# Optimization experiments

Hardware: AMD Instinct MI355X
Metric: run time of the kernel (lower is better)

## Reference

```python
import jax, jax.numpy as jnp
import numpy as np

EMB = 1024
HEADS = 16
DK = EMB // HEADS
EPS = 1e-5


def setup_inputs() -> dict:
    key = jax.random.key(0)
    ks = jax.random.split(key, 7)
    s_in = 1.0 / np.sqrt(EMB)
    return {
        "x": jax.random.normal(ks[0], (4, 2048, EMB), dtype=jnp.float32),
        "W_qkv": jax.random.uniform(ks[1], (EMB, 3 * EMB), jnp.float32, -s_in, s_in),
        "b_qkv": jax.random.uniform(ks[2], (3 * EMB,), jnp.float32, -s_in, s_in),
        "W_out": jax.random.uniform(ks[3], (EMB, EMB), jnp.float32, -s_in, s_in),
        "b_out": jax.random.uniform(ks[4], (EMB,), jnp.float32, -s_in, s_in),
        "gamma": jnp.ones((EMB,), jnp.float32),
        "beta": jnp.zeros((EMB,), jnp.float32),
    }


def reference(x, W_qkv, b_qkv, W_out, b_out, gamma, beta):
    B, T, D = x.shape
    qkv = x @ W_qkv + b_qkv                      # [B,T,3D]
    q, k, v = jnp.split(qkv, 3, axis=-1)
    # [B,T,D] -> [B,H,T,dk]
    def heads(t):
        return t.reshape(B, T, HEADS, DK).transpose(0, 2, 1, 3)
    q, k, v = heads(q), heads(k), heads(v)
    scores = jnp.einsum("bhtd,bhsd->bhts", q, k) / np.sqrt(DK)
    attn = jax.nn.softmax(scores, axis=-1)
    out = jnp.einsum("bhts,bhsd->bhtd", attn, v)  # [B,H,T,dk]
    out = out.transpose(0, 2, 1, 3).reshape(B, T, D)
    out = out @ W_out + b_out
    res = x + out
    mu = jnp.mean(res, axis=-1, keepdims=True)
    var = jnp.mean((res - mu) ** 2, axis=-1, keepdims=True)
    return (res - mu) / jnp.sqrt(var + EPS) * gamma + beta
```

## Files before the change

kernel.cpp:

```cpp
#include <hip/hip_runtime.h>

#define B_ 4
#define T_ 2048
#define D_ 1024
#define H_ 16
#define DK_ 64
#define M_ (B_*T_)

typedef __bf16 bf16;
typedef __bf16 bf16x8 __attribute__((ext_vector_type(8)));
typedef __bf16 bf16x4 __attribute__((ext_vector_type(4)));
typedef short s16x4 __attribute__((ext_vector_type(4)));
typedef float f32x4 __attribute__((ext_vector_type(4)));

__device__ __forceinline__ f32x4 zero4() { f32x4 v = {0.f, 0.f, 0.f, 0.f}; return v; }

__device__ __forceinline__ float fexp2(float x) {
  float r;
  asm("v_exp_f32 %0, %1\n\ts_nop 0" : "=v"(r) : "v"(x));
  return r;
}

__device__ __forceinline__ float max3f(float a, float b, float c) {
  float r;
  asm("v_max3_f32 %0, %1, %2, %3" : "=v"(r) : "v"(a), "v"(b), "v"(c));
  return r;
}

__device__ __forceinline__ void g2l16(const void* g, void* l) {
  __builtin_amdgcn_global_load_lds(
      (const __attribute__((address_space(1))) void*)g,
      (__attribute__((address_space(3))) void*)l, 16, 0, 0);
}

__global__ __launch_bounds__(256) void cast_bf16(const float* __restrict__ src,
                                                 bf16* __restrict__ dst) {
  const size_t i = ((size_t)blockIdx.x * 256 + threadIdx.x) * 8;
  float4 a = *(const float4*)(src + i);
  float4 b = *(const float4*)(src + i + 4);
  bf16x8 v;
  v[0] = (bf16)a.x; v[1] = (bf16)a.y; v[2] = (bf16)a.z; v[3] = (bf16)a.w;
  v[4] = (bf16)b.x; v[5] = (bf16)b.y; v[6] = (bf16)b.z; v[7] = (bf16)b.w;
  *(bf16x8*)(dst + i) = v;
}

__global__ __launch_bounds__(256) void transpose_wf(const float* __restrict__ src,
                                                    bf16* __restrict__ dst, int R, int C) {
  __shared__ alignas(16) bf16 ts[64 * 65];
  const int tid = threadIdx.x;
  const int r0 = blockIdx.x * 64, c0 = blockIdx.y * 64;
  {
    int rr = tid >> 2, cc = (tid & 3) * 16;
    const float4* p4 = (const float4*)(src + (size_t)(r0 + rr) * C + c0 + cc);
    float fv[16];
#pragma unroll
    for (int q = 0; q < 4; ++q) *(float4*)&fv[q * 4] = p4[q];
#pragma unroll
    for (int i = 0; i < 16; ++i) ts[(cc + i) * 65 + rr] = (bf16)fv[i];
  }
  __syncthreads();
  {
    int rr = tid >> 2, cc = (tid & 3) * 16;
    bf16x8 a, b;
#pragma unroll
    for (int i = 0; i < 8; ++i) a[i] = ts[rr * 65 + cc + i];
#pragma unroll
    for (int i = 0; i < 8; ++i) b[i] = ts[rr * 65 + cc + 8 + i];
    bf16* q = dst + (size_t)(c0 + rr) * R + r0 + cc;
    *(bf16x8*)q = a;
    *(bf16x8*)(q + 8) = b;
  }
}

template <bool FUSE>
__global__ __launch_bounds__(256) void gemm64(const bf16* __restrict__ A,
                                              const bf16* __restrict__ Bt,
                                              const float* __restrict__ bias,
                                              bf16* __restrict__ Cbf,
                                              float* __restrict__ Cf,
                                              const float* __restrict__ resid,
                                              int N, int K, int lda, int ldc) {
  __shared__ alignas(16) bf16 As[128 * 64];
  __shared__ alignas(16) bf16 Bs[128 * 64];
  const int tid = threadIdx.x;
  const int wid = tid >> 6, lane = tid & 63, quad = lane >> 4, l16 = lane & 15;
  const int m0 = blockIdx.x * 128, n0 = blockIdx.y * 128;
  const int wr = (wid >> 1) * 64, wc = (wid & 1) * 64;
  const int sw = l16 & 7;

  f32x4 acc[4][4];
#pragma unroll
  for (int i = 0; i < 4; ++i)
#pragma unroll
    for (int j = 0; j < 4; ++j) acc[i][j] = zero4();

  for (int k0 = 0; k0 < K; k0 += 64) {
    __syncthreads();
#pragma unroll
    for (int p = 0; p < 4; ++p) {
      const int t = p * 256 + tid;
      const int row = t >> 3;
      const int kcs = ((t & 7) ^ (row & 7)) * 8;
      g2l16(Bt + (size_t)(n0 + row) * K + k0 + kcs, (char*)Bs + p * 4096 + wid * 1024);
      g2l16(A + (size_t)(m0 + row) * lda + k0 + kcs, (char*)As + p * 4096 + wid * 1024);
    }
    __syncthreads();
#pragma unroll
    for (int kk = 0; kk < 2; ++kk) {
      bf16x8 af[4], bfr[4];
#pragma unroll
      for (int i = 0; i < 4; ++i)
        af[i] = *(const bf16x8*)&As[(wr + i * 16 + l16) * 64 + ((((kk << 2) | quad) ^ sw) * 8)];
#pragma unroll
      for (int j = 0; j < 4; ++j)
        bfr[j] = *(const bf16x8*)&Bs[(wc + j * 16 + l16) * 64 + ((((kk << 2) | quad) ^ sw) * 8)];
#pragma unroll
      for (int i = 0; i < 4; ++i)
#pragma unroll
        for (int j = 0; j < 4; ++j)
          acc[i][j] = __builtin_amdgcn_mfma_f32_16x16x32_bf16(af[i], bfr[j], acc[i][j], 0, 0, 0);
    }
  }

#pragma unroll
  for (int i = 0; i < 4; ++i) {
#pragma unroll
    for (int j = 0; j < 4; ++j) {
      const int col = n0 + wc + j * 16 + l16;
      const float bv = bias[col];
#pragma unroll
      for (int r = 0; r < 4; ++r) {
        const int row = m0 + wr + i * 16 + quad * 4 + r;
        const float v = acc[i][j][r] + bv;
        if (FUSE) {
          const size_t off = (size_t)row * N + col;
          Cf[off] = v + resid[off];
        } else {
          Cbf[(size_t)row * ldc + col] = (bf16)v;
        }
      }
    }
  }
}

__global__ __launch_bounds__(256, 4) void attn_db(const bf16* __restrict__ qkv,
                                                  bf16* __restrict__ ao) {
  __shared__ alignas(16) bf16 Ks[2][4096];
  __shared__ alignas(16) bf16 Vs2[2][4096];
  const int tid = threadIdx.x;
  const int wid = tid >> 6, lane = tid & 63, quad = lane >> 4, l16 = lane & 15;
  const int bid0 = blockIdx.x;
  const int bid = ((bid0 & 7) << 7) | (bid0 >> 3);
  const int qb = bid & 15, h = (bid >> 4) & 15, b = bid >> 8;
  const int q0 = qb * 128;

  const int lrow8 = lane >> 3;
  const int kch = (lane & 7) ^ lrow8;
  const bf16* kg = qkv + (size_t)(b * T_ + wid * 16 + lrow8) * (3 * D_) + D_ + h * DK_ + kch * 8;
  const int vtok = wid * 8 + (lane >> 5) * 4 + ((lane >> 1) & 3);
  const int vfof = ((lane >> 3) & 3) * 16 + (lane & 1) * 8;
  const bf16* vg = qkv + (size_t)(b * T_ + vtok) * (3 * D_) + 2 * D_ + h * DK_ + vfof;
  const unsigned vbase = (unsigned)(uintptr_t)&Vs2[0][0];

  const float SC = 0.125f * 1.44269504f;
  bf16x8 qA[2], qB[2];
  {
    const bf16* qpA = qkv + (size_t)(b * T_ + q0 + wid * 32 + l16) * (3 * D_) + h * DK_ + quad * 8;
    const bf16* qpB = qpA + (size_t)16 * (3 * D_);
    qA[0] = *(const bf16x8*)qpA;       qA[1] = *(const bf16x8*)(qpA + 32);
    qB[0] = *(const bf16x8*)qpB;       qB[1] = *(const bf16x8*)(qpB + 32);
#pragma unroll
    for (int i = 0; i < 8; ++i) {
      qA[0][i] = (bf16)((float)qA[0][i] * SC); qA[1][i] = (bf16)((float)qA[1][i] * SC);
      qB[0][i] = (bf16)((float)qB[0][i] * SC); qB[1][i] = (bf16)((float)qB[1][i] * SC);
    }
  }

  float miA = -1e30f, miB = -1e30f;
  f32x4 liA4 = zero4(), liB4 = zero4();
  f32x4 oA[4], oB[4];
#pragma unroll
  for (int ft = 0; ft < 4; ++ft) { oA[ft] = zero4(); oB[ft] = zero4(); }

  auto stage = [&](int buf, int t0) {
    g2l16(kg + (size_t)(t0 + 0) * (3 * D_), &Ks[buf][(wid * 16 + 0) * 64]);
    g2l16(kg + (size_t)(t0 + 8) * (3 * D_), &Ks[buf][(wid * 16 + 8) * 64]);
    g2l16(vg + (size_t)(t0 + 0) * (3 * D_),  (char*)&Vs2[buf][0] + (0 + wid * 2) * 512);
    g2l16(vg + (size_t)(t0 + 32) * (3 * D_), (char*)&Vs2[buf][0] + (8 + wid * 2) * 512);
  };

  stage(0, 0);
  __syncthreads();

  for (int kt = 0; kt < T_ / 64; ++kt) {
    const int cur = kt & 1;
    if (kt + 1 < T_ / 64) stage(cur ^ 1, (kt + 1) * 64);

    f32x4 svA[4], svB[4];
#pragma unroll
    for (int nt = 0; nt < 4; ++nt) { svA[nt] = zero4(); svB[nt] = zero4(); }
    __builtin_amdgcn_s_setprio(1);
#pragma unroll
    for (int nt = 0; nt < 4; ++nt)
#pragma unroll
      for (int ks = 0; ks < 2; ++ks) {
        const bf16x8 kf = *(const bf16x8*)
            &Ks[cur][(nt * 16 + l16) * 64 + (((ks << 2) | quad) ^ (l16 & 7)) * 8];
        svA[nt] = __builtin_amdgcn_mfma_f32_16x16x32_bf16(kf, qA[ks], svA[nt], 0, 0, 0);
        svB[nt] = __builtin_amdgcn_mfma_f32_16x16x32_bf16(kf, qB[ks], svB[nt], 0, 0, 0);
      }
    __builtin_amdgcn_s_setprio(0);

    float a0 = max3f(svA[0][0], svA[0][1], svA[0][2]);
    float a1 = max3f(svA[0][3], svA[1][0], svA[1][1]);
    a0 = max3f(a0, svA[1][2], svA[1][3]);
    a1 = max3f(a1, svA[2][0], svA[2][1]);
    a0 = max3f(a0, svA[2][2], svA[2][3]);
    a1 = max3f(a1, svA[3][0], svA[3][1]);
    a0 = max3f(a0, svA[3][2], svA[3][3]);
    float b0 = max3f(svB[0][0], svB[0][1], svB[0][2]);
    float b1 = max3f(svB[0][3], svB[1][0], svB[1][1]);
    b0 = max3f(b0, svB[1][2], svB[1][3]);
    b1 = max3f(b1, svB[2][0], svB[2][1]);
    b0 = max3f(b0, svB[2][2], svB[2][3]);
    b1 = max3f(b1, svB[3][0], svB[3][1]);
    b0 = max3f(b0, svB[3][2], svB[3][3]);
    const float tAl = fmaxf(a0, a1), tBl = fmaxf(b0, b1);

    if (!__all(tAl <= miA + 8.f)) {
      float tA = fmaxf(tAl, __shfl_xor(tAl, 16, 64));
      tA = fmaxf(tA, __shfl_xor(tA, 32, 64));
      const float nm = fmaxf(miA, tA);
      const float al = fexp2(miA - nm);
      miA = nm; liA4 *= al;
#pragma unroll
      for (int r = 0; r < 4; ++r) {
        const float ar = __shfl(al, quad * 4 + r, 64);
#pragma unroll
        for (int ft = 0; ft < 4; ++ft) oA[ft][r] *= ar;
      }
    }
    if (!__all(tBl <= miB + 8.f)) {
      float tB = fmaxf(tBl, __shfl_xor(tBl, 16, 64));
      tB = fmaxf(tB, __shfl_xor(tB, 32, 64));
      const float nm = fmaxf(miB, tB);
      const float al = fexp2(miB - nm);
      miB = nm; liB4 *= al;
#pragma unroll
      for (int r = 0; r < 4; ++r) {
        const float ar = __shfl(al, quad * 4 + r, 64);
#pragma unroll
        for (int ft = 0; ft < 4; ++ft) oB[ft][r] *= ar;
      }
    }

    s16x4 pA[4], pB[4];
#pragma unroll
    for (int nt = 0; nt < 4; ++nt) {
      f32x4 dA = svA[nt] - miA;
      dA[0] = fexp2(dA[0]); dA[1] = fexp2(dA[1]); dA[2] = fexp2(dA[2]); dA[3] = fexp2(dA[3]);
      liA4 += dA;
      union { bf16x4 b; s16x4 s; } ua;
#pragma unroll
      for (int j = 0; j < 4; ++j) ua.b[j] = (bf16)dA[j];
      pA[nt] = ua.s;
      f32x4 dB = svB[nt] - miB;
      dB[0] = fexp2(dB[0]); dB[1] = fexp2(dB[1]); dB[2] = fexp2(dB[2]); dB[3] = fexp2(dB[3]);
      liB4 += dB;
      union { bf16x4 b; s16x4 s; } ub;
#pragma unroll
      for (int j = 0; j < 4; ++j) ub.b[j] = (bf16)dB[j];
      pB[nt] = ub.s;
    }

    __builtin_amdgcn_s_setprio(1);
    {
      const unsigned va = vbase + (unsigned)cur * 8192u + (unsigned)(quad * 512 + l16 * 8);
#pragma unroll
      for (int ks = 0; ks < 4; ++ks) {
        s16x4 vf[4];
#pragma unroll
        for (int ft = 0; ft < 4; ++ft)
          asm volatile("ds_read_b64_tr_b16 %0, %1 offset:%2"
                       : "=v"(vf[ft]) : "v"(va), "i"(ks * 2048 + ft * 128));
        asm volatile("s_waitcnt lgkmcnt(0)" ::: "memory");
        __builtin_amdgcn_sched_barrier(0);
#pragma unroll
        for (int ft = 0; ft < 4; ++ft) {
          oA[ft] = __builtin_amdgcn_mfma_f32_16x16x16bf16_1k(pA[ks], vf[ft], oA[ft], 0, 0, 0);
          oB[ft] = __builtin_amdgcn_mfma_f32_16x16x16bf16_1k(pB[ks], vf[ft], oB[ft], 0, 0, 0);
        }
      }
    }
    __builtin_amdgcn_s_setprio(0);

    __syncthreads();
  }

  float sA = (liA4[0] + liA4[1]) + (liA4[2] + liA4[3]);
  sA += __shfl_xor(sA, 16, 64);
  sA += __shfl_xor(sA, 32, 64);
  float sB = (liB4[0] + liB4[1]) + (liB4[2] + liB4[3]);
  sB += __shfl_xor(sB, 16, 64);
  sB += __shfl_xor(sB, 32, 64);

#pragma unroll
  for (int r = 0; r < 4; ++r) {
    const float invA = 1.0f / __shfl(sA, quad * 4 + r, 64);
    const float invB = 1.0f / __shfl(sB, quad * 4 + r, 64);
    const int rowA = b * T_ + q0 + wid * 32 + quad * 4 + r;
    const int rowB = rowA + 16;
#pragma unroll
    for (int ft = 0; ft < 4; ++ft) {
      ao[(size_t)rowA * D_ + h * DK_ + ft * 16 + l16] = (bf16)(oA[ft][r] * invA);
      ao[(size_t)rowB * D_ + h * DK_ + ft * 16 + l16] = (bf16)(oB[ft][r] * invB);
    }
  }
}

__global__ __launch_bounds__(256) void ln_out(float* __restrict__ res,
                                              const float* __restrict__ gamma,
                                              const float* __restrict__ beta) {
  const int row = blockIdx.x * 4 + (threadIdx.x >> 6);
  const int lane = threadIdx.x & 63;
  float4 v[4];
  float s = 0.f, q = 0.f;
#pragma unroll
  for (int p = 0; p < 4; ++p) {
    v[p] = *(const float4*)(res + (size_t)row * D_ + p * 256 + lane * 4);
    s += v[p].x + v[p].y + v[p].z + v[p].w;
    q += v[p].x * v[p].x + v[p].y * v[p].y + v[p].z * v[p].z + v[p].w * v[p].w;
  }
#pragma unroll
  for (int m = 1; m < 64; m <<= 1) { s += __shfl_xor(s, m, 64); q += __shfl_xor(q, m, 64); }
  const float mu = s * (1.0f / D_);
  const float var = q * (1.0f / D_) - mu * mu;
  const float rstd = rsqrtf(var + 1e-5f);
#pragma unroll
  for (int p = 0; p < 4; ++p) {
    const int c = p * 256 + lane * 4;
    const float4 g = *(const float4*)(gamma + c);
    const float4 be = *(const float4*)(beta + c);
    float4 ov;
    ov.x = (v[p].x - mu) * rstd * g.x + be.x;
    ov.y = (v[p].y - mu) * rstd * g.y + be.y;
    ov.z = (v[p].z - mu) * rstd * g.z + be.z;
    ov.w = (v[p].w - mu) * rstd * g.w + be.w;
    *(float4*)(res + (size_t)row * D_ + c) = ov;
  }
}

extern "C" void kernel_launch(void* const* d_in, const int* in_sizes, int n_in,
                              void* d_out, int out_size, void* d_ws, size_t ws_size,
                              hipStream_t stream) {
  const float* x     = (const float*)d_in[0];
  const float* Wqkv  = (const float*)d_in[1];
  const float* bqkv  = (const float*)d_in[2];
  const float* Wout  = (const float*)d_in[3];
  const float* bout  = (const float*)d_in[4];
  const float* gamma = (const float*)d_in[5];
  const float* beta  = (const float*)d_in[6];
  float* out = (float*)d_out;

  char* ws = (char*)d_ws;
  bf16* WqkvT = (bf16*)ws; ws += (size_t)3 * D_ * D_ * 2;
  bf16* WoutT = (bf16*)ws; ws += (size_t)D_ * D_ * 2;
  bf16* qkv   = (bf16*)ws; ws += (size_t)M_ * 3 * D_ * 2;
  bf16* ao    = (bf16*)ws;
  bf16* xb    = ao;

  transpose_wf<<<dim3(D_ / 64, 3 * D_ / 64), 256, 0, stream>>>(Wqkv, WqkvT, D_, 3 * D_);
  transpose_wf<<<dim3(D_ / 64, D_ / 64), 256, 0, stream>>>(Wout, WoutT, D_, D_);
  cast_bf16<<<M_ * D_ / (256 * 8), 256, 0, stream>>>(x, xb);
  gemm64<false><<<dim3(M_ / 128, 3 * D_ / 128), 256, 0, stream>>>(
      xb, WqkvT, bqkv, qkv, nullptr, nullptr, 3 * D_, D_, D_, 3 * D_);
  attn_db<<<B_ * H_ * (T_ / 128), 256, 0, stream>>>(qkv, ao);
  gemm64<true><<<dim3(M_ / 128, D_ / 128), 256, 0, stream>>>(
      ao, WoutT, bout, nullptr, out, x, D_, D_, D_, D_);
  ln_out<<<M_ / 4, 256, 0, stream>>>(out, gamma, beta);
}
```

Measured before the change: 298.1 us.

## Merge prep kernels into one launch and remap GEMM blocks for XCD locality

The cast of x and the two weight transposes become a single `prep` kernel that dispatches on block index, which removes two kernel launches. Both GEMMs switch to a 1D grid with a remapping that spreads consecutive block IDs across 8 groups (XCD-style swizzle). This is meant to keep tiles that share data on the same L2. The remap hardcodes 64 M-tiles and assumes the grid size is divisible by 8.

```diff
diff --git a/kernel.cpp b/kernel.cpp
--- a/kernel.cpp
+++ b/kernel.cpp
@@ -33,22 +33,29 @@
       (__attribute__((address_space(3))) void*)l, 16, 0, 0);
 }
 
-__global__ __launch_bounds__(256) void cast_bf16(const float* __restrict__ src,
-                                                 bf16* __restrict__ dst) {
-  const size_t i = ((size_t)blockIdx.x * 256 + threadIdx.x) * 8;
-  float4 a = *(const float4*)(src + i);
-  float4 b = *(const float4*)(src + i + 4);
-  bf16x8 v;
-  v[0] = (bf16)a.x; v[1] = (bf16)a.y; v[2] = (bf16)a.z; v[3] = (bf16)a.w;
-  v[4] = (bf16)b.x; v[5] = (bf16)b.y; v[6] = (bf16)b.z; v[7] = (bf16)b.w;
-  *(bf16x8*)(dst + i) = v;
-}
-
-__global__ __launch_bounds__(256) void transpose_wf(const float* __restrict__ src,
-                                                    bf16* __restrict__ dst, int R, int C) {
+__global__ __launch_bounds__(256) void prep(const float* __restrict__ x,
+                                            const float* __restrict__ Wqkv,
+                                            const float* __restrict__ Wout,
+                                            bf16* __restrict__ xb,
+                                            bf16* __restrict__ WqkvT,
+                                            bf16* __restrict__ WoutT) {
   __shared__ alignas(16) bf16 ts[64 * 65];
+  const int id = blockIdx.x;
   const int tid = threadIdx.x;
-  const int r0 = blockIdx.x * 64, c0 = blockIdx.y * 64;
+  if (id < 4096) {
+    const size_t i = ((size_t)id * 256 + tid) * 8;
+    float4 a = *(const float4*)(x + i);
+    float4 b = *(const float4*)(x + i + 4);
+    bf16x8 v;
+    v[0] = (bf16)a.x; v[1] = (bf16)a.y; v[2] = (bf16)a.z; v[3] = (bf16)a.w;
+    v[4] = (bf16)b.x; v[5] = (bf16)b.y; v[6] = (bf16)b.z; v[7] = (bf16)b.w;
+    *(bf16x8*)(xb + i) = v;
+    return;
+  }
+  const float* src; bf16* dst; int C, t;
+  if (id < 4096 + 768) { t = id - 4096; src = Wqkv; dst = WqkvT; C = 3 * D_; }
+  else                 { t = id - 4864; src = Wout; dst = WoutT; C = D_; }
+  const int r0 = (t & 15) * 64, c0 = (t >> 4) * 64;
   {
     int rr = tid >> 2, cc = (tid & 3) * 16;
     const float4* p4 = (const float4*)(src + (size_t)(r0 + rr) * C + c0 + cc);
@@ -66,7 +73,7 @@
     for (int i = 0; i < 8; ++i) a[i] = ts[rr * 65 + cc + i];
 #pragma unroll
     for (int i = 0; i < 8; ++i) b[i] = ts[rr * 65 + cc + 8 + i];
-    bf16* q = dst + (size_t)(c0 + rr) * R + r0 + cc;
+    bf16* q = dst + (size_t)(c0 + rr) * D_ + r0 + cc;
     *(bf16x8*)q = a;
     *(bf16x8*)(q + 8) = b;
   }
@@ -84,7 +91,8 @@
   __shared__ alignas(16) bf16 Bs[128 * 64];
   const int tid = threadIdx.x;
   const int wid = tid >> 6, lane = tid & 63, quad = lane >> 4, l16 = lane & 15;
-  const int m0 = blockIdx.x * 128, n0 = blockIdx.y * 128;
+  const int w = (blockIdx.x & 7) * (gridDim.x >> 3) + (blockIdx.x >> 3);
+  const int m0 = (w & 63) * 128, n0 = (w >> 6) * 128;
   const int wr = (wid >> 1) * 64, wc = (wid & 1) * 64;
   const int sw = l16 & 7;
 
@@ -369,13 +377,11 @@
   bf16* ao    = (bf16*)ws;
   bf16* xb    = ao;
 
-  transpose_wf<<<dim3(D_ / 64, 3 * D_ / 64), 256, 0, stream>>>(Wqkv, WqkvT, D_, 3 * D_);
-  transpose_wf<<<dim3(D_ / 64, D_ / 64), 256, 0, stream>>>(Wout, WoutT, D_, D_);
-  cast_bf16<<<M_ * D_ / (256 * 8), 256, 0, stream>>>(x, xb);
-  gemm64<false><<<dim3(M_ / 128, 3 * D_ / 128), 256, 0, stream>>>(
+  prep<<<4096 + 768 + 256, 256, 0, stream>>>(x, Wqkv, Wout, xb, WqkvT, WoutT);
+  gemm64<false><<<(M_ / 128) * (3 * D_ / 128), 256, 0, stream>>>(
       xb, WqkvT, bqkv, qkv, nullptr, nullptr, 3 * D_, D_, D_, 3 * D_);
   attn_db<<<B_ * H_ * (T_ / 128), 256, 0, stream>>>(qkv, ao);
-  gemm64<true><<<dim3(M_ / 128, D_ / 128), 256, 0, stream>>>(
+  gemm64<true><<<(M_ / 128) * (D_ / 128), 256, 0, stream>>>(
       ao, WoutT, bout, nullptr, out, x, D_, D_, D_, D_);
   ln_out<<<M_ / 4, 256, 0, stream>>>(out, gamma, beta);
 }
```

Result: slower. 304.8 us (+2.2%).
